# Optimization experiments

Hardware: AMD Instinct MI355X
Metric: run time of the kernel (lower is better)

Reference implementation:

```python
import jax, jax.numpy as jnp
import numpy as np

B = 4096
IND = 512
OUTD = 512
DEG = 2
P = 2  # dim_treat
KNOTS = [[0.33, 0.66], [0.33, 0.66]]
D = DEG + 1 + len(KNOTS[0])  # 5 basis functions per treatment dim


def setup_inputs() -> dict:
    key = jax.random.key(0)
    k1, k2, k3 = jax.random.split(key, 3)
    x = jax.random.uniform(k1, (B, P + IND), dtype=jnp.float32)  # treat dims in [0,1]
    weight = jax.random.uniform(k2, (IND, OUTD, D ** P), dtype=jnp.float32)  # torch.rand init
    bias = jax.random.uniform(k3, (OUTD, D ** P), dtype=jnp.float32)
    return {"x": x, "weight": weight, "bias": bias}


def _truncated_power_basis(x_treat):
    # x_treat: [B, P] -> basis: [B, P, D]
    knots = jnp.asarray(KNOTS, dtype=x_treat.dtype)  # [P, n_knots]
    # polynomial part: 1, x, x^2, ... x^DEG
    pows = jnp.stack([x_treat ** i for i in range(DEG + 1)], axis=-1)  # [B, P, DEG+1]
    # truncated part: relu(x - knot)^DEG  (DEG > 1 branch of original code)
    trunc = jax.nn.relu(x_treat[:, :, None] - knots[None, :, :]) ** DEG  # [B, P, n_knots]
    return jnp.concatenate([pows, trunc], axis=-1)


def reference(x, weight, bias):
    x_treat = x[:, :P]          # [B, P]
    x_feature = x[:, P:]        # [B, IND]
    basis = _truncated_power_basis(x_treat)  # [B, P, D]
    # Kronecker product across the two treatment dims: outer product, flattened
    kb = jnp.einsum('bi,bj->bij', basis[:, 0, :], basis[:, 1, :]).reshape(x.shape[0], D * P * 0 + D * D)  # [B, D^2]
    # fused: (weight^T @ x_feature) contracted with the per-sample basis coefficients
    out = jnp.einsum('bi,iod,bd->bo', x_feature, weight, kb)  # [B, OUTD]
    out = out + kb @ bias.T      # bias also varies with treatment basis
    out = jax.nn.relu(out)       # act='relu'
    # islastlayer=0: re-attach treatment dims
    return jnp.concatenate([x_treat, out], axis=1)  # [B, P + OUTD]
```

## Files before the change

kernel.cpp:

```cpp
#include <hip/hip_runtime.h>
#include <hip/hip_bf16.h>
#include <string.h>

#define NB    4096
#define IND_  512
#define OUTD_ 512
#define XCOLS 514
#define ND    25
#define KTOT  12800

#define WT_DS   262144
#define WT_BIAS 6553600

#define BM 32
#define BN 128

#define PWI 64
#define PWO 4
#define PWC (PWO * ND)
#define T8P 112

typedef float  f32x4  __attribute__((ext_vector_type(4)));
typedef int    i32x4  __attribute__((ext_vector_type(4)));
typedef int    i32x8  __attribute__((ext_vector_type(8)));
typedef unsigned int   u32x2 __attribute__((ext_vector_type(2)));

__device__ __forceinline__ unsigned char f2fp8(float v) {
  if (v < 0.015625f) {
    return (unsigned char)__float2int_rn(v * 512.0f);
  }
  unsigned int u = __float_as_uint(v);
  u += 0x7ffffu + ((u >> 20) & 1u);
  int e = (int)(u >> 23) - 127 + 7;
  unsigned int m = (u >> 20) & 7u;
  return (unsigned char)((e << 3) | m);
}

__device__ __forceinline__ float basis_f(float t, int j) {
  switch (j) {
    case 0: return 1.0f;
    case 1: return t;
    case 2: return t * t;
    case 3: { float r = t - 0.33f; r = r > 0.0f ? r : 0.0f; return r * r; }
    default:{ float r = t - 0.66f; r = r > 0.0f ? r : 0.0f; return r * r; }
  }
}

__global__ __launch_bounds__(256) void prep_all_kernel(
    const float* __restrict__ x, const float* __restrict__ W,
    const float* __restrict__ bias, unsigned char* __restrict__ Xf8,
    float* __restrict__ kbDT, unsigned char* __restrict__ kbT8,
    unsigned char* __restrict__ Wt, float* __restrict__ out)
{
  __shared__ unsigned char tile8[PWI * T8P];
  const int bid = blockIdx.x;
  const int tid = threadIdx.x;

  if (bid < 512) {
    const int lane = tid & 63;
    #pragma unroll
    for (int rr = 0; rr < 2; ++rr) {
      const int b = bid * 8 + (tid >> 6) * 2 + rr;
      const float* xr = x + (size_t)b * XCOLS;
      const float* fp = xr + 2 + lane * 8;
      float2 a0 = *(const float2*)(fp + 0);
      float2 a1 = *(const float2*)(fp + 2);
      float2 a2 = *(const float2*)(fp + 4);
      float2 a3 = *(const float2*)(fp + 6);
      float xf[8] = {a0.x, a0.y, a1.x, a1.y, a2.x, a2.y, a3.x, a3.y};
      u32x2 pk;
      pk[0] = (unsigned int)f2fp8(xf[0]) | ((unsigned int)f2fp8(xf[1]) << 8) |
              ((unsigned int)f2fp8(xf[2]) << 16) | ((unsigned int)f2fp8(xf[3]) << 24);
      pk[1] = (unsigned int)f2fp8(xf[4]) | ((unsigned int)f2fp8(xf[5]) << 8) |
              ((unsigned int)f2fp8(xf[6]) << 16) | ((unsigned int)f2fp8(xf[7]) << 24);
      *reinterpret_cast<u32x2*>(Xf8 + (size_t)b * IND_ + lane * 8) = pk;

      float t0 = xr[0], t1 = xr[1];
      if (lane < 2) out[(size_t)b * XCOLS + lane] = (lane == 0) ? t0 : t1;
      {
        int d1 = lane / 5, d2 = lane - d1 * 5;
        float kvd = basis_f(t0, d1) * basis_f(t1, d2);
        float kvn = 0.0f;
        if (lane < 24) {
          int e1 = (lane + 1) / 5, e2 = (lane + 1) - e1 * 5;
          kvn = basis_f(t0, e1) * basis_f(t1, e2);
        }
        if (lane < ND) {
          int bt = b >> 7, bl = b & 15, nf = (b >> 4) & 7;
          kbDT[(((size_t)lane * 32 + bt) * 16 + bl) * 8 + nf] = kvd - kvn;
        }
      }
      {
        int ta = 2 * lane, tb = 2 * lane + 1;
        unsigned char ba = 0, bb = 0;
        if (ta < ND) { int d1 = ta / 5, d2 = ta - d1 * 5;
                       ba = f2fp8(basis_f(t0, d1) * basis_f(t1, d2)); }
        if (tb < ND) { int d1 = tb / 5, d2 = tb - d1 * 5;
                       bb = f2fp8(basis_f(t0, d1) * basis_f(t1, d2)); }
        *(unsigned short*)(kbT8 + (size_t)b * 128 + 2 * lane) =
            (unsigned short)ba | ((unsigned short)bb << 8);
      }
    }
  } else {
    const int pw = bid - 512;
    const int i0 = (pw & 7) * PWI;
    const int o0 = (pw >> 3) * PWO;

    for (int t = tid; t < PWI * (PWC / 4); t += 256) {
      int il = t / (PWC / 4);
      int c4 = t - il * (PWC / 4);
      float4 v = *(const float4*)(W + ((size_t)(i0 + il) * OUTD_ + o0) * ND + c4 * 4);
      unsigned int pk = (unsigned int)f2fp8(v.x) | ((unsigned int)f2fp8(v.y) << 8) |
                        ((unsigned int)f2fp8(v.z) << 16) | ((unsigned int)f2fp8(v.w) << 24);
      *(unsigned int*)&tile8[il * T8P + c4 * 4] = pk;
    }
    __syncthreads();

    for (int g = tid; g < PWC * (PWI / 8); g += 256) {
      int c  = g >> 3;
      int ig = g & 7;
      int d  = c % 25;
      int o_l = c / 25;
      unsigned long long v = 0;
      #pragma unroll
      for (int jj = 0; jj < 8; ++jj)
        v |= (unsigned long long)tile8[(ig * 8 + jj) * T8P + c] << (8 * jj);
      int o  = o0 + o_l;
      int ib = i0 + ig * 8;
      int iw = ib >> 7;
      int wb = ib & 127;
      size_t dest = (((size_t)d * 32 + (o >> 4)) * 4 + iw) * 2048
                  + (size_t)(((wb >> 5) * 16 + (o & 15)) * 32 + (wb & 31));
      *reinterpret_cast<unsigned long long*>(Wt + dest) = v;
    }

    if ((pw & 7) == 0) {
      int o = o0 + (tid >> 6);
      int p = tid & 63;
      int ta = 2 * p, tb = 2 * p + 1;
      unsigned char ba = (ta < ND) ? f2fp8(bias[o * ND + ta]) : (unsigned char)0;
      unsigned char bb = (tb < ND) ? f2fp8(bias[o * ND + tb]) : (unsigned char)0;
      size_t dest = WT_BIAS + (size_t)(o >> 4) * 2048
                  + (size_t)(((ta >> 5) * 16 + (o & 15)) * 32 + (ta & 31));
      *(unsigned short*)(Wt + dest) =
          (unsigned short)ba | ((unsigned short)bb << 8);
    }
  }
}

__global__ __launch_bounds__(256, 3) void gemm_out_kernel(
    const unsigned char* __restrict__ Wt, const unsigned char* __restrict__ Xf8,
    const float* __restrict__ kbDT, const unsigned char* __restrict__ kbT8,
    float* __restrict__ out)
{
  const int tid  = threadIdx.x;
  const int lane = tid & 63;
  const int w    = tid >> 6;
  const int l15  = lane & 15;
  const int quad = lane >> 4;

  const int id = blockIdx.x;
  const int ox = ((id & 7) << 1) | ((id >> 3) & 1);
  const int by = id >> 4;

  const int o0 = ox * BM;
  const int b0 = by * BN;

  const int og = ox * 2 + (w >> 1);
  const int bh = w & 1;

  auto load8 = [](const unsigned char* p) -> i32x8 {
    i32x4 lo = *reinterpret_cast<const i32x4*>(p);
    i32x4 hi = *reinterpret_cast<const i32x4*>(p + 16);
    i32x8 v;
    v[0] = lo[0]; v[1] = lo[1]; v[2] = lo[2]; v[3] = lo[3];
    v[4] = hi[0]; v[5] = hi[1]; v[6] = hi[2]; v[7] = hi[3];
    return v;
  };

  f32x4 fin[4];
  #pragma unroll
  for (int nf = 0; nf < 4; ++nf) fin[nf] = (f32x4)0.0f;

  const float* dBase = kbDT + (((size_t)by * 16 + l15) * 8) + bh * 4;

  for (int iw = 0; iw < 4; ++iw) {
    i32x8 bfr[4];
    #pragma unroll
    for (int nf = 0; nf < 4; ++nf)
      bfr[nf] = load8(Xf8 + (size_t)(b0 + bh * 64 + nf * 16 + l15) * IND_
                          + iw * 128 + quad * 32);

    const unsigned char* aP = Wt + ((size_t)og * 4 + iw) * 2048 + lane * 32;
    const float* dP = dBase;

    f32x4 acc[4];
    #pragma unroll
    for (int nf = 0; nf < 4; ++nf) acc[nf] = (f32x4)0.0f;

    auto mfma_flush = [&](const i32x8& a, const f32x4& q) {
      #pragma unroll
      for (int nf = 0; nf < 4; ++nf)
        acc[nf] = __builtin_amdgcn_mfma_scale_f32_16x16x128_f8f6f4(
            a, bfr[nf], acc[nf], 0, 0, 0, 0x7f7f7f7f, 0, 0x7f7f7f7f);
      #pragma unroll
      for (int nf = 0; nf < 4; ++nf)
        #pragma unroll
        for (int r = 0; r < 4; ++r)
          fin[nf][r] += q[nf] * acc[nf][r];
    };

    i32x8 a0 = load8(aP);
    i32x8 a1 = load8(aP + WT_DS);
    i32x8 a2;
    f32x4 qA = *reinterpret_cast<const f32x4*>(dP);
    f32x4 qB, qC;

    for (int pass = 0; pass < 8; ++pass) {
      a2 = load8(aP + 2 * WT_DS);
      qB = *reinterpret_cast<const f32x4*>(dP + 4096);
      mfma_flush(a0, qA);

      a0 = load8(aP + 3 * WT_DS);
      qC = *reinterpret_cast<const f32x4*>(dP + 8192);
      mfma_flush(a1, qB);

      a1 = load8(aP + 4 * WT_DS);
      qA = *reinterpret_cast<const f32x4*>(dP + 12288);
      mfma_flush(a2, qC);

      aP += 3 * WT_DS;
      dP += 12288;
    }

    mfma_flush(a0, qA);
  }

  {
    i32x8 ab = load8(Wt + WT_BIAS + (size_t)og * 2048 + lane * 32);
    i32x8 bft[4];
    #pragma unroll
    for (int nf = 0; nf < 4; ++nf)
      bft[nf] = load8(kbT8 + (size_t)(b0 + bh * 64 + nf * 16 + l15) * 128
                           + quad * 32);
    #pragma unroll
    for (int nf = 0; nf < 4; ++nf)
      fin[nf] = __builtin_amdgcn_mfma_scale_f32_16x16x128_f8f6f4(
          ab, bft[nf], fin[nf], 0, 0, 0, 0x7f7f7f7f, 0, 0x7f7f7f7f);
  }

  #pragma unroll
  for (int nf = 0; nf < 4; ++nf) {
    int bg = b0 + bh * 64 + nf * 16 + l15;
    int oo = o0 + (w >> 1) * 16 + quad * 4;
    float* op = out + (size_t)bg * XCOLS + 2 + oo;
    float2 lo, hi;
    lo.x = fin[nf][0] > 0.0f ? fin[nf][0] : 0.0f;
    lo.y = fin[nf][1] > 0.0f ? fin[nf][1] : 0.0f;
    hi.x = fin[nf][2] > 0.0f ? fin[nf][2] : 0.0f;
    hi.y = fin[nf][3] > 0.0f ? fin[nf][3] : 0.0f;
    *(float2*)op = lo;
    *(float2*)(op + 2) = hi;
  }
}

extern "C" void kernel_launch(void* const* d_in, const int* in_sizes, int n_in,
                              void* d_out, int out_size, void* d_ws, size_t ws_size,
                              hipStream_t stream) {
  const float* x    = (const float*)d_in[0];
  const float* W    = (const float*)d_in[1];
  const float* bias = (const float*)d_in[2];
  float* out = (float*)d_out;
  char* ws = (char*)d_ws;

  const size_t xf_off  = 0;
  const size_t wf_off  = 2097152;
  const size_t kb_off  = wf_off + 6619136;
  const size_t kbt_off = kb_off + 409600;
  unsigned char* Xf8  = (unsigned char*)(ws + xf_off);
  unsigned char* Wt   = (unsigned char*)(ws + wf_off);
  float* kbDT         = (float*)(ws + kb_off);
  unsigned char* kbT8 = (unsigned char*)(ws + kbt_off);

  prep_all_kernel<<<1536, 256, 0, stream>>>(x, W, bias, Xf8, kbDT, kbT8, Wt, out);
  gemm_out_kernel<<<512, 256, 0, stream>>>(Wt, Xf8, kbDT, kbT8, out);
}
```

Baseline: 123.6 us.

## Replace telescoping accumulator with ping-pong zero-init MFMA buffers per basis term

The GEMM previously chained all 25 basis-term MFMAs through one running accumulator and scaled it by differences of consecutive basis coefficients (kv_d - kv_{d+1}). Every flush therefore had to wait on the latest MFMA, and every next MFMA had to wait on the same accumulator. Now each basis term's MFMAs start from zero into one of two alternating accumulator sets, A and B, and are scaled by the raw coefficient kv_d. This lets MFMAs for one term overlap with the scalar FMA flush of the previous term. The prep kernel now stores kv directly instead of the difference, at the cost of a second accumulator set and more register pressure.

```diff
diff --git a/kernel.cpp b/kernel.cpp
--- a/kernel.cpp
+++ b/kernel.cpp
@@ -49,7 +49,7 @@
 __global__ __launch_bounds__(256) void prep_all_kernel(
     const float* __restrict__ x, const float* __restrict__ W,
     const float* __restrict__ bias, unsigned char* __restrict__ Xf8,
-    float* __restrict__ kbDT, unsigned char* __restrict__ kbT8,
+    float* __restrict__ kbKV, unsigned char* __restrict__ kbT8,
     unsigned char* __restrict__ Wt, float* __restrict__ out)
 {
   __shared__ unsigned char tile8[PWI * T8P];
@@ -80,14 +80,9 @@
       {
         int d1 = lane / 5, d2 = lane - d1 * 5;
         float kvd = basis_f(t0, d1) * basis_f(t1, d2);
-        float kvn = 0.0f;
-        if (lane < 24) {
-          int e1 = (lane + 1) / 5, e2 = (lane + 1) - e1 * 5;
-          kvn = basis_f(t0, e1) * basis_f(t1, e2);
-        }
         if (lane < ND) {
           int bt = b >> 7, bl = b & 15, nf = (b >> 4) & 7;
-          kbDT[(((size_t)lane * 32 + bt) * 16 + bl) * 8 + nf] = kvd - kvn;
+          kbKV[(((size_t)lane * 32 + bt) * 16 + bl) * 8 + nf] = kvd;
         }
       }
       {
@@ -150,7 +145,7 @@
 
 __global__ __launch_bounds__(256, 3) void gemm_out_kernel(
     const unsigned char* __restrict__ Wt, const unsigned char* __restrict__ Xf8,
-    const float* __restrict__ kbDT, const unsigned char* __restrict__ kbT8,
+    const float* __restrict__ kbKV, const unsigned char* __restrict__ kbT8,
     float* __restrict__ out)
 {
   const int tid  = threadIdx.x;
@@ -182,7 +177,8 @@
   #pragma unroll
   for (int nf = 0; nf < 4; ++nf) fin[nf] = (f32x4)0.0f;
 
-  const float* dBase = kbDT + (((size_t)by * 16 + l15) * 8) + bh * 4;
+  const f32x4 Z = (f32x4)0.0f;
+  const float* dBase = kbKV + (((size_t)by * 16 + l15) * 8) + bh * 4;
 
   for (int iw = 0; iw < 4; ++iw) {
     i32x8 bfr[4];
@@ -194,46 +190,56 @@
     const unsigned char* aP = Wt + ((size_t)og * 4 + iw) * 2048 + lane * 32;
     const float* dP = dBase;
 
-    f32x4 acc[4];
-    #pragma unroll
-    for (int nf = 0; nf < 4; ++nf) acc[nf] = (f32x4)0.0f;
-
-    auto mfma_flush = [&](const i32x8& a, const f32x4& q) {
-      #pragma unroll
-      for (int nf = 0; nf < 4; ++nf)
-        acc[nf] = __builtin_amdgcn_mfma_scale_f32_16x16x128_f8f6f4(
-            a, bfr[nf], acc[nf], 0, 0, 0, 0x7f7f7f7f, 0, 0x7f7f7f7f);
+    f32x4 accA[4], accB[4];
+    auto mfma4A = [&](const i32x8& a) {
+      #pragma unroll
+      for (int nf = 0; nf < 4; ++nf)
+        accA[nf] = __builtin_amdgcn_mfma_scale_f32_16x16x128_f8f6f4(
+            a, bfr[nf], Z, 0, 0, 0, 0x7f7f7f7f, 0, 0x7f7f7f7f);
+    };
+    auto mfma4B = [&](const i32x8& a) {
+      #pragma unroll
+      for (int nf = 0; nf < 4; ++nf)
+        accB[nf] = __builtin_amdgcn_mfma_scale_f32_16x16x128_f8f6f4(
+            a, bfr[nf], Z, 0, 0, 0, 0x7f7f7f7f, 0, 0x7f7f7f7f);
+    };
+    auto flushA = [&](const f32x4& q) {
       #pragma unroll
       for (int nf = 0; nf < 4; ++nf)
         #pragma unroll
         for (int r = 0; r < 4; ++r)
-          fin[nf][r] += q[nf] * acc[nf][r];
+          fin[nf][r] += q[nf] * accA[nf][r];
+    };
+    auto flushB = [&](const f32x4& q) {
+      #pragma unroll
+      for (int nf = 0; nf < 4; ++nf)
+        #pragma unroll
+        for (int r = 0; r < 4; ++r)
+          fin[nf][r] += q[nf] * accB[nf][r];
     };
 
     i32x8 a0 = load8(aP);
     i32x8 a1 = load8(aP + WT_DS);
-    i32x8 a2;
     f32x4 qA = *reinterpret_cast<const f32x4*>(dP);
-    f32x4 qB, qC;
-
-    for (int pass = 0; pass < 8; ++pass) {
-      a2 = load8(aP + 2 * WT_DS);
-      qB = *reinterpret_cast<const f32x4*>(dP + 4096);
-      mfma_flush(a0, qA);
-
-      a0 = load8(aP + 3 * WT_DS);
-      qC = *reinterpret_cast<const f32x4*>(dP + 8192);
-      mfma_flush(a1, qB);
-
-      a1 = load8(aP + 4 * WT_DS);
-      qA = *reinterpret_cast<const f32x4*>(dP + 12288);
-      mfma_flush(a2, qC);
-
-      aP += 3 * WT_DS;
-      dP += 12288;
-    }
-
-    mfma_flush(a0, qA);
+    f32x4 qB = *reinterpret_cast<const f32x4*>(dP + 4096);
+
+    mfma4A(a0);
+    a0 = load8(aP + 2 * WT_DS);
+
+    for (int p = 0; p < 12; ++p) {
+      mfma4B(a1);
+      a1 = load8(aP + 3 * WT_DS);
+      f32x4 qC = *reinterpret_cast<const f32x4*>(dP + 2 * 4096);
+      flushA(qA);
+      mfma4A(a0);
+      a0 = load8(aP + 4 * WT_DS);
+      f32x4 qD = *reinterpret_cast<const f32x4*>(dP + 3 * 4096);
+      flushB(qB);
+      qA = qC; qB = qD;
+      aP += 2 * WT_DS;
+      dP += 2 * 4096;
+    }
+    flushA(qA);
   }
 
   {
@@ -279,9 +285,9 @@
   const size_t kbt_off = kb_off + 409600;
   unsigned char* Xf8  = (unsigned char*)(ws + xf_off);
   unsigned char* Wt   = (unsigned char*)(ws + wf_off);
-  float* kbDT         = (float*)(ws + kb_off);
+  float* kbKV         = (float*)(ws + kb_off);
   unsigned char* kbT8 = (unsigned char*)(ws + kbt_off);
 
-  prep_all_kernel<<<1536, 256, 0, stream>>>(x, W, bias, Xf8, kbDT, kbT8, Wt, out);
-  gemm_out_kernel<<<512, 256, 0, stream>>>(Wt, Xf8, kbDT, kbT8, out);
-}
+  prep_all_kernel<<<1536, 256, 0, stream>>>(x, W, bias, Xf8, kbKV, kbT8, Wt, out);
+  gemm_out_kernel<<<512, 256, 0, stream>>>(Wt, Xf8, kbKV, kbT8, out);
+}
```

Result: faster. 118.4 us (-4.2%).
